# Performance work log

Hardware: AMD Instinct MI355X
Metric: run time of the kernel (lower is better)

Reference implementation:

```python
import jax, jax.numpy as jnp
import numpy as np

EMBED_DIM = 256
UNITS = 512


def setup_inputs() -> dict:
    key = jax.random.key(0)
    k1, k2, k3, k4, k5, k6, k7, k8 = jax.random.split(key, 8)
    B, L = 2048, 64
    features = jax.random.normal(k1, (B, L, EMBED_DIM), dtype=jnp.float32)
    hidden = jax.random.normal(k2, (B, UNITS), dtype=jnp.float32)
    s1 = 1.0 / np.sqrt(EMBED_DIM)
    s2 = 1.0 / np.sqrt(UNITS)
    W1 = jax.random.normal(k3, (EMBED_DIM, UNITS), dtype=jnp.float32) * s1
    b1 = jnp.zeros((UNITS,), dtype=jnp.float32)
    W2 = jax.random.normal(k4, (UNITS, UNITS), dtype=jnp.float32) * s2
    b2 = jnp.zeros((UNITS,), dtype=jnp.float32)
    V = jax.random.normal(k5, (UNITS, 1), dtype=jnp.float32) * s2
    bV = jnp.zeros((1,), dtype=jnp.float32)
    return {"features": features, "hidden": hidden, "W1": W1, "b1": b1,
            "W2": W2, "b2": b2, "V": V, "bV": bV}


def reference(features, hidden, W1, b1, W2, b2, V, bV):
    # features: [B, L, D_feat]; hidden: [B, U]
    # score = tanh(W1(features) + W2(hidden)[:, None])  -> [B, L, U]
    proj_f = jnp.einsum('bld,du->blu', features, W1) + b1
    proj_h = hidden @ W2 + b2                         # [B, U]
    score = jnp.tanh(proj_f + proj_h[:, None, :])     # [B, L, U]
    logits = jnp.einsum('blu,uo->blo', score, V) + bV  # [B, L, 1]
    attention_weights = jax.nn.softmax(logits, axis=1)  # softmax over L
    context_vector = jnp.sum(attention_weights * features, axis=1)  # [B, D_feat]
    return context_vector, attention_weights
```

## Files before the change

kernel.cpp:

```cpp
#include <hip/hip_runtime.h>
#include <math.h>

#define B_N 2048
#define L_N 64
#define D_N 256
#define U_N 512

typedef __attribute__((ext_vector_type(8))) short bf16x8;
typedef __attribute__((ext_vector_type(4))) float f32x4;

__device__ __forceinline__ float fast_tanh(float x) {
    float e = __builtin_amdgcn_exp2f(x * 2.8853900817779268f);
    float r = __builtin_amdgcn_rcpf(e + 1.0f);
    return fmaf(-2.0f, r, 1.0f);
}
__device__ __forceinline__ ushort f2bf(float x) {
    uint b = __float_as_uint(x);
    uint r = (b + 0x7FFF + ((b >> 16) & 1)) >> 16;
    return (ushort)r;
}
__device__ __forceinline__ float bf2f(ushort u) {
    uint v = ((uint)u) << 16;
    return __uint_as_float(v);
}

__global__ __launch_bounds__(256) void pack_weights(
    const float* __restrict__ W1, const float* __restrict__ W2,
    ushort* __restrict__ W1p, ushort* __restrict__ W2p)
{
    ushort tmp[8];
    if (blockIdx.x < 64) {
        int g = blockIdx.x * 256 + threadIdx.x;
        int ntg = g >> 9, ks = (g >> 6) & 7, lane = g & 63;
        int n  = ntg * 16 + (lane & 15);
        int kb = ks * 32 + (lane >> 4) * 8;
#pragma unroll
        for (int j = 0; j < 8; ++j) tmp[j] = f2bf(W1[(kb + j) * U_N + n]);
        *(uint4*)&W1p[(size_t)g * 8] = *(uint4*)tmp;
    } else {
        int g = (blockIdx.x - 64) * 256 + threadIdx.x;
        int ntg = g >> 10, ks = (g >> 6) & 15, lane = g & 63;
        int n  = ntg * 16 + (lane & 15);
        int kb = ks * 32 + (lane >> 4) * 8;
#pragma unroll
        for (int j = 0; j < 8; ++j) tmp[j] = f2bf(W2[(kb + j) * U_N + n]);
        *(uint4*)&W2p[(size_t)g * 8] = *(uint4*)tmp;
    }
}

__global__ __launch_bounds__(256) void proj_h_mfma(
    const float* __restrict__ hidden, const ushort* __restrict__ W2p,
    const float* __restrict__ b1, const float* __restrict__ b2,
    ushort* __restrict__ ph)
{
    __shared__ ushort As[16 * 512];

    const int t  = threadIdx.x;
    const int b0 = blockIdx.x * 16;
    const int u0 = blockIdx.y * 128;

#pragma unroll
    for (int i = 0; i < 4; ++i) {
        int f = t + i * 256;
        int m = f >> 6, c = f & 63;
        float4 x0 = *(const float4*)&hidden[(b0 + m) * U_N + c * 8];
        float4 x1 = *(const float4*)&hidden[(b0 + m) * U_N + c * 8 + 4];
        ushort tmp[8] = {f2bf(x0.x), f2bf(x0.y), f2bf(x0.z), f2bf(x0.w),
                         f2bf(x1.x), f2bf(x1.y), f2bf(x1.z), f2bf(x1.w)};
        *(uint4*)&As[(m * 64 + (c ^ (m & 7))) * 8] = *(uint4*)tmp;
    }
    __syncthreads();

    const int w = t >> 6, lane = t & 63;
    const int ml = lane & 15, q = lane >> 4;

    f32x4 acc[2];
#pragma unroll
    for (int nt = 0; nt < 2; ++nt) acc[nt] = (f32x4){0.f, 0.f, 0.f, 0.f};

    for (int ks = 0; ks < 16; ++ks) {
        int c = ks * 4 + q;
        bf16x8 a = *(const bf16x8*)&As[(ml * 64 + (c ^ (ml & 7))) * 8];
        bf16x8 bb[2];
#pragma unroll
        for (int nt = 0; nt < 2; ++nt) {
            int ntg = blockIdx.y * 8 + w * 2 + nt;
            bb[nt] = *(const bf16x8*)&W2p[(size_t)((ntg * 16 + ks) * 64 + lane) * 8];
        }
#pragma unroll
        for (int nt = 0; nt < 2; ++nt)
            acc[nt] = __builtin_amdgcn_mfma_f32_16x16x32_bf16(a, bb[nt], acc[nt], 0, 0, 0);
    }

#pragma unroll
    for (int nt = 0; nt < 2; ++nt) {
        int n = u0 + (w * 2 + nt) * 16 + ml;
        float bias = b1[n] + b2[n];
#pragma unroll
        for (int r = 0; r < 4; ++r)
            ph[(size_t)(b0 + q * 4 + r) * U_N + n] = f2bf(acc[nt][r] + bias);
    }
}

__global__ __launch_bounds__(256) void attn_kernel(
    const float* __restrict__ features, const ushort* __restrict__ W1p,
    const float* __restrict__ V, const float* __restrict__ bV,
    const ushort* __restrict__ ph, float* __restrict__ out)
{
    __shared__ ushort As[64 * 256];
    __shared__ float lpart[4][64];
    __shared__ float wls[64];

    const int b    = blockIdx.x;
    const int t    = threadIdx.x;
    const int w    = t >> 6;
    const int lane = t & 63;
    const int ml   = lane & 15;
    const int q    = lane >> 4;
    const float* fb = features + (size_t)b * (L_N * D_N);

#pragma unroll
    for (int i = 0; i < 8; ++i) {
        int f = t + i * 256;
        int m = f >> 5, c = f & 31;
        float4 x0 = *(const float4*)&fb[m * D_N + c * 8];
        float4 x1 = *(const float4*)&fb[m * D_N + c * 8 + 4];
        ushort tmp[8] = {f2bf(x0.x), f2bf(x0.y), f2bf(x0.z), f2bf(x0.w),
                         f2bf(x1.x), f2bf(x1.y), f2bf(x1.z), f2bf(x1.w)};
        *(uint4*)&As[(m * 32 + (c ^ (m & 31))) * 8] = *(uint4*)tmp;
    }
    __syncthreads();

    float lp[16];
#pragma unroll
    for (int j = 0; j < 16; ++j) lp[j] = 0.f;

    const ushort* W1w = W1p + (size_t)(w * 8) * 8 * 64 * 8;

    for (int uc = 0; uc < 4; ++uc) {
        f32x4 acc[4][2];
#pragma unroll
        for (int mt = 0; mt < 4; ++mt)
#pragma unroll
            for (int nt = 0; nt < 2; ++nt)
                acc[mt][nt] = (f32x4){0.f, 0.f, 0.f, 0.f};

        bf16x8 bfc[2], bfn[2];
#pragma unroll
        for (int nt = 0; nt < 2; ++nt)
            bfc[nt] = *(const bf16x8*)&W1w[(size_t)(((uc * 2 + nt) * 8 + 0) * 64 + lane) * 8];

        for (int ks = 0; ks < 8; ++ks) {
            if (ks < 7) {
#pragma unroll
                for (int nt = 0; nt < 2; ++nt)
                    bfn[nt] = *(const bf16x8*)&W1w[(size_t)(((uc * 2 + nt) * 8 + ks + 1) * 64 + lane) * 8];
            }
            bf16x8 a[4];
#pragma unroll
            for (int mt = 0; mt < 4; ++mt) {
                int m = mt * 16 + ml;
                int c = ks * 4 + q;
                a[mt] = *(const bf16x8*)&As[(m * 32 + (c ^ (m & 31))) * 8];
            }
#pragma unroll
            for (int nt = 0; nt < 2; ++nt)
#pragma unroll
                for (int mt = 0; mt < 4; ++mt)
                    acc[mt][nt] = __builtin_amdgcn_mfma_f32_16x16x32_bf16(
                        a[mt], bfc[nt], acc[mt][nt], 0, 0, 0);
            bfc[0] = bfn[0]; bfc[1] = bfn[1];
        }

#pragma unroll
        for (int nt = 0; nt < 2; ++nt) {
            int n = w * 128 + uc * 32 + nt * 16 + ml;
            float phv = bf2f(ph[(size_t)b * U_N + n]);
            float vv  = V[n];
#pragma unroll
            for (int mt = 0; mt < 4; ++mt)
#pragma unroll
                for (int r = 0; r < 4; ++r) {
                    float s = fast_tanh(acc[mt][nt][r] + phv);
                    lp[mt * 4 + r] = fmaf(s, vv, lp[mt * 4 + r]);
                }
        }
    }

#pragma unroll
    for (int off = 1; off <= 8; off <<= 1)
#pragma unroll
        for (int j = 0; j < 16; ++j)
            lp[j] += __shfl_xor(lp[j], off);
    if (ml == 0) {
#pragma unroll
        for (int mt = 0; mt < 4; ++mt)
#pragma unroll
            for (int r = 0; r < 4; ++r)
                lpart[w][mt * 16 + q * 4 + r] = lp[mt * 4 + r];
    }
    __syncthreads();

    if (t < 64) {
        float lsum = bV[0] + lpart[0][t] + lpart[1][t] + lpart[2][t] + lpart[3][t];
        float mx = lsum;
#pragma unroll
        for (int off = 32; off > 0; off >>= 1)
            mx = fmaxf(mx, __shfl_xor(mx, off));
        float e = __expf(lsum - mx);
        float ssum = e;
#pragma unroll
        for (int off = 32; off > 0; off >>= 1)
            ssum += __shfl_xor(ssum, off);
        float wt = e / ssum;
        wls[t] = wt;
        out[(size_t)B_N * D_N + (size_t)b * L_N + t] = wt;
    }
    __syncthreads();

    float ctx = 0.f;
#pragma unroll 16
    for (int l = 0; l < L_N; ++l) {
        ushort u = As[(l * 32 + ((t >> 3) ^ (l & 31))) * 8 + (t & 7)];
        ctx = fmaf(wls[l], bf2f(u), ctx);
    }
    out[(size_t)b * D_N + t] = ctx;
}

extern "C" void kernel_launch(void* const* d_in, const int* in_sizes, int n_in,
                              void* d_out, int out_size, void* d_ws, size_t ws_size,
                              hipStream_t stream) {
    const float* features = (const float*)d_in[0];
    const float* hidden   = (const float*)d_in[1];
    const float* W1       = (const float*)d_in[2];
    const float* b1       = (const float*)d_in[3];
    const float* W2       = (const float*)d_in[4];
    const float* b2       = (const float*)d_in[5];
    const float* V        = (const float*)d_in[6];
    const float* bV       = (const float*)d_in[7];
    float* out = (float*)d_out;

    ushort* ph  = (ushort*)d_ws;
    ushort* W1p = (ushort*)((char*)d_ws + (size_t)B_N * U_N * 2);
    ushort* W2p = (ushort*)((char*)d_ws + (size_t)B_N * U_N * 2 + (size_t)D_N * U_N * 2);

    pack_weights<<<192, 256, 0, stream>>>(W1, W2, W1p, W2p);
    proj_h_mfma<<<dim3(B_N / 16, U_N / 128), 256, 0, stream>>>(hidden, W2p, b1, b2, ph);
    attn_kernel<<<B_N, 256, 0, stream>>>(features, W1p, V, bV, ph, out);
}
```

Baseline: 262.8 us.

## Process several batches per block with double-buffered feature prefetch

Each attention block now handles four batch rows in turn. The features for the next row are loaded into registers while the current row's MFMA work runs, then written to a second LDS buffer, so global-load latency overlaps with compute. The W1 fragment prefetch is also deepened to two k-steps ahead. In exchange, LDS use doubles to 64KB per block, register pressure rises (16 float4 prefetch registers, with launch bounds set for 2 blocks per CU), and the grid shrinks to 512 blocks, which may leave compute units underfilled.

```diff
diff --git a/kernel.cpp b/kernel.cpp
--- a/kernel.cpp
+++ b/kernel.cpp
@@ -5,6 +5,7 @@
 #define L_N 64
 #define D_N 256
 #define U_N 512
+#define NB  4
 
 typedef __attribute__((ext_vector_type(8))) short bf16x8;
 typedef __attribute__((ext_vector_type(4))) float f32x4;
@@ -102,129 +103,164 @@
     }
 }
 
-__global__ __launch_bounds__(256) void attn_kernel(
+__global__ __launch_bounds__(256, 2) void attn_kernel(
     const float* __restrict__ features, const ushort* __restrict__ W1p,
     const float* __restrict__ V, const float* __restrict__ bV,
     const ushort* __restrict__ ph, float* __restrict__ out)
 {
-    __shared__ ushort As[64 * 256];
+    __shared__ ushort As[2][64 * 256];
     __shared__ float lpart[4][64];
     __shared__ float wls[64];
 
-    const int b    = blockIdx.x;
     const int t    = threadIdx.x;
     const int w    = t >> 6;
     const int lane = t & 63;
     const int ml   = lane & 15;
     const int q    = lane >> 4;
-    const float* fb = features + (size_t)b * (L_N * D_N);
-
-#pragma unroll
-    for (int i = 0; i < 8; ++i) {
-        int f = t + i * 256;
-        int m = f >> 5, c = f & 31;
-        float4 x0 = *(const float4*)&fb[m * D_N + c * 8];
-        float4 x1 = *(const float4*)&fb[m * D_N + c * 8 + 4];
-        ushort tmp[8] = {f2bf(x0.x), f2bf(x0.y), f2bf(x0.z), f2bf(x0.w),
-                         f2bf(x1.x), f2bf(x1.y), f2bf(x1.z), f2bf(x1.w)};
-        *(uint4*)&As[(m * 32 + (c ^ (m & 31))) * 8] = *(uint4*)tmp;
-    }
+    const int b0   = blockIdx.x * NB;
+
+    float4 pf[16];
+
+#define ISSUE(bb) do {                                                        \
+        const float* fb_ = features + (size_t)(bb) * (L_N * D_N);             \
+        _Pragma("unroll")                                                     \
+        for (int i = 0; i < 8; ++i) {                                         \
+            int f_ = t + i * 256;                                             \
+            int m_ = f_ >> 5, c_ = f_ & 31;                                   \
+            pf[2*i]   = *(const float4*)&fb_[m_ * D_N + c_ * 8];              \
+            pf[2*i+1] = *(const float4*)&fb_[m_ * D_N + c_ * 8 + 4];          \
+        }                                                                     \
+    } while (0)
+
+#define WRITE(buf) do {                                                       \
+        _Pragma("unroll")                                                     \
+        for (int i = 0; i < 8; ++i) {                                         \
+            int f_ = t + i * 256;                                             \
+            int m_ = f_ >> 5, c_ = f_ & 31;                                   \
+            float4 x0_ = pf[2*i], x1_ = pf[2*i+1];                            \
+            ushort tmp_[8] = {f2bf(x0_.x), f2bf(x0_.y), f2bf(x0_.z), f2bf(x0_.w), \
+                              f2bf(x1_.x), f2bf(x1_.y), f2bf(x1_.z), f2bf(x1_.w)}; \
+            *(uint4*)&As[buf][(m_ * 32 + (c_ ^ (m_ & 31))) * 8] = *(uint4*)tmp_;  \
+        }                                                                     \
+    } while (0)
+
+    ISSUE(b0);
+    WRITE(0);
     __syncthreads();
 
-    float lp[16];
-#pragma unroll
-    for (int j = 0; j < 16; ++j) lp[j] = 0.f;
-
     const ushort* W1w = W1p + (size_t)(w * 8) * 8 * 64 * 8;
-
-    for (int uc = 0; uc < 4; ++uc) {
-        f32x4 acc[4][2];
-#pragma unroll
-        for (int mt = 0; mt < 4; ++mt)
-#pragma unroll
-            for (int nt = 0; nt < 2; ++nt)
-                acc[mt][nt] = (f32x4){0.f, 0.f, 0.f, 0.f};
-
-        bf16x8 bfc[2], bfn[2];
-#pragma unroll
-        for (int nt = 0; nt < 2; ++nt)
-            bfc[nt] = *(const bf16x8*)&W1w[(size_t)(((uc * 2 + nt) * 8 + 0) * 64 + lane) * 8];
-
-        for (int ks = 0; ks < 8; ++ks) {
-            if (ks < 7) {
+    int cur = 0;
+
+    for (int bi = 0; bi < NB; ++bi) {
+        const int b = b0 + bi;
+
+        if (bi + 1 < NB) ISSUE(b + 1);
+        __builtin_amdgcn_sched_barrier(0);
+
+        float lp[16];
+#pragma unroll
+        for (int j = 0; j < 16; ++j) lp[j] = 0.f;
+
+        for (int uc = 0; uc < 4; ++uc) {
+            f32x4 acc[4][2];
+#pragma unroll
+            for (int mt = 0; mt < 4; ++mt)
 #pragma unroll
                 for (int nt = 0; nt < 2; ++nt)
-                    bfn[nt] = *(const bf16x8*)&W1w[(size_t)(((uc * 2 + nt) * 8 + ks + 1) * 64 + lane) * 8];
+                    acc[mt][nt] = (f32x4){0.f, 0.f, 0.f, 0.f};
+
+            bf16x8 bf0[2], bf1[2], bfn[2];
+#pragma unroll
+            for (int nt = 0; nt < 2; ++nt) {
+                bf0[nt] = *(const bf16x8*)&W1w[(size_t)(((uc * 2 + nt) * 8 + 0) * 64 + lane) * 8];
+                bf1[nt] = *(const bf16x8*)&W1w[(size_t)(((uc * 2 + nt) * 8 + 1) * 64 + lane) * 8];
             }
-            bf16x8 a[4];
-#pragma unroll
-            for (int mt = 0; mt < 4; ++mt) {
-                int m = mt * 16 + ml;
-                int c = ks * 4 + q;
-                a[mt] = *(const bf16x8*)&As[(m * 32 + (c ^ (m & 31))) * 8];
+
+            for (int ks = 0; ks < 8; ++ks) {
+                if (ks < 6) {
+#pragma unroll
+                    for (int nt = 0; nt < 2; ++nt)
+                        bfn[nt] = *(const bf16x8*)&W1w[(size_t)(((uc * 2 + nt) * 8 + ks + 2) * 64 + lane) * 8];
+                }
+                bf16x8 a[4];
+#pragma unroll
+                for (int mt = 0; mt < 4; ++mt) {
+                    int m = mt * 16 + ml;
+                    int c = ks * 4 + q;
+                    a[mt] = *(const bf16x8*)&As[cur][(m * 32 + (c ^ (m & 31))) * 8];
+                }
+#pragma unroll
+                for (int nt = 0; nt < 2; ++nt)
+#pragma unroll
+                    for (int mt = 0; mt < 4; ++mt)
+                        acc[mt][nt] = __builtin_amdgcn_mfma_f32_16x16x32_bf16(
+                            a[mt], bf0[nt], acc[mt][nt], 0, 0, 0);
+                bf0[0] = bf1[0]; bf0[1] = bf1[1];
+                bf1[0] = bfn[0]; bf1[1] = bfn[1];
             }
-#pragma unroll
-            for (int nt = 0; nt < 2; ++nt)
+
+#pragma unroll
+            for (int nt = 0; nt < 2; ++nt) {
+                int n = w * 128 + uc * 32 + nt * 16 + ml;
+                float phv = bf2f(ph[(size_t)b * U_N + n]);
+                float vv  = V[n];
 #pragma unroll
                 for (int mt = 0; mt < 4; ++mt)
-                    acc[mt][nt] = __builtin_amdgcn_mfma_f32_16x16x32_bf16(
-                        a[mt], bfc[nt], acc[mt][nt], 0, 0, 0);
-            bfc[0] = bfn[0]; bfc[1] = bfn[1];
-        }
-
-#pragma unroll
-        for (int nt = 0; nt < 2; ++nt) {
-            int n = w * 128 + uc * 32 + nt * 16 + ml;
-            float phv = bf2f(ph[(size_t)b * U_N + n]);
-            float vv  = V[n];
+#pragma unroll
+                    for (int r = 0; r < 4; ++r) {
+                        float s = fast_tanh(acc[mt][nt][r] + phv);
+                        lp[mt * 4 + r] = fmaf(s, vv, lp[mt * 4 + r]);
+                    }
+            }
+        }
+
+#pragma unroll
+        for (int off = 1; off <= 8; off <<= 1)
+#pragma unroll
+            for (int j = 0; j < 16; ++j)
+                lp[j] += __shfl_xor(lp[j], off);
+
+        __syncthreads();
+        if (bi + 1 < NB) WRITE(cur ^ 1);
+
+        if (ml == 0) {
 #pragma unroll
             for (int mt = 0; mt < 4; ++mt)
 #pragma unroll
-                for (int r = 0; r < 4; ++r) {
-                    float s = fast_tanh(acc[mt][nt][r] + phv);
-                    lp[mt * 4 + r] = fmaf(s, vv, lp[mt * 4 + r]);
-                }
-        }
-    }
-
-#pragma unroll
-    for (int off = 1; off <= 8; off <<= 1)
-#pragma unroll
-        for (int j = 0; j < 16; ++j)
-            lp[j] += __shfl_xor(lp[j], off);
-    if (ml == 0) {
-#pragma unroll
-        for (int mt = 0; mt < 4; ++mt)
-#pragma unroll
-            for (int r = 0; r < 4; ++r)
-                lpart[w][mt * 16 + q * 4 + r] = lp[mt * 4 + r];
-    }
-    __syncthreads();
-
-    if (t < 64) {
-        float lsum = bV[0] + lpart[0][t] + lpart[1][t] + lpart[2][t] + lpart[3][t];
-        float mx = lsum;
-#pragma unroll
-        for (int off = 32; off > 0; off >>= 1)
-            mx = fmaxf(mx, __shfl_xor(mx, off));
-        float e = __expf(lsum - mx);
-        float ssum = e;
-#pragma unroll
-        for (int off = 32; off > 0; off >>= 1)
-            ssum += __shfl_xor(ssum, off);
-        float wt = e / ssum;
-        wls[t] = wt;
-        out[(size_t)B_N * D_N + (size_t)b * L_N + t] = wt;
-    }
-    __syncthreads();
-
-    float ctx = 0.f;
+                for (int r = 0; r < 4; ++r)
+                    lpart[w][mt * 16 + q * 4 + r] = lp[mt * 4 + r];
+        }
+        __syncthreads();
+
+        if (t < 64) {
+            float lsum = bV[0] + lpart[0][t] + lpart[1][t] + lpart[2][t] + lpart[3][t];
+            float mx = lsum;
+#pragma unroll
+            for (int off = 32; off > 0; off >>= 1)
+                mx = fmaxf(mx, __shfl_xor(mx, off));
+            float e = __expf(lsum - mx);
+            float ssum = e;
+#pragma unroll
+            for (int off = 32; off > 0; off >>= 1)
+                ssum += __shfl_xor(ssum, off);
+            float wt = e / ssum;
+            wls[t] = wt;
+            out[(size_t)B_N * D_N + (size_t)b * L_N + t] = wt;
+        }
+        __syncthreads();
+
+        float ctx = 0.f;
 #pragma unroll 16
-    for (int l = 0; l < L_N; ++l) {
-        ushort u = As[(l * 32 + ((t >> 3) ^ (l & 31))) * 8 + (t & 7)];
-        ctx = fmaf(wls[l], bf2f(u), ctx);
-    }
-    out[(size_t)b * D_N + t] = ctx;
+        for (int l = 0; l < L_N; ++l) {
+            ushort u = As[cur][(l * 32 + ((t >> 3) ^ (l & 31))) * 8 + (t & 7)];
+            ctx = fmaf(wls[l], bf2f(u), ctx);
+        }
+        out[(size_t)b * D_N + t] = ctx;
+
+        cur ^= 1;
+    }
+#undef ISSUE
+#undef WRITE
 }
 
 extern "C" void kernel_launch(void* const* d_in, const int* in_sizes, int n_in,
@@ -246,5 +282,5 @@
 
     pack_weights<<<192, 256, 0, stream>>>(W1, W2, W1p, W2p);
     proj_h_mfma<<<dim3(B_N / 16, U_N / 128), 256, 0, stream>>>(hidden, W2p, b1, b2, ph);
-    attn_kernel<<<B_N, 256, 0, stream>>>(features, W1p, V, bV, ph, out);
-}
+    attn_kernel<<<B_N / NB, 256, 0, stream>>>(features, W1p, V, bV, ph, out);
+}
```

Measured after the change: 307.1 us. 16.8% more time.

## Pre-convert features to bf16 and double-buffer async LDS loads across batches

Applied to the files above, without the earlier changes.

Feature conversion to bf16 moves into the prep kernel, which writes a packed bf16 copy to the workspace. The attention kernel now handles 4 batches per block, prefetching the next batch's features into a second LDS buffer with global_load_lds while computing the current one. It also widens the per-wave N tile to 4 MFMA columns and fixes waves per EU at 2. The aim is to hide feature-load latency, at the cost of extra global traffic for the intermediate bf16 copy and doubled LDS.

```diff
diff --git a/kernel.cpp b/kernel.cpp
--- a/kernel.cpp
+++ b/kernel.cpp
@@ -5,6 +5,7 @@
 #define L_N 64
 #define D_N 256
 #define U_N 512
+#define NB  4
 
 typedef __attribute__((ext_vector_type(8))) short bf16x8;
 typedef __attribute__((ext_vector_type(4))) float f32x4;
@@ -24,27 +25,50 @@
     return __uint_as_float(v);
 }
 
-__global__ __launch_bounds__(256) void pack_weights(
+__device__ __forceinline__ void gll16(const ushort* g, ushort* l) {
+    __builtin_amdgcn_global_load_lds(
+        (const __attribute__((address_space(1))) unsigned int*)g,
+        (__attribute__((address_space(3))) unsigned int*)l,
+        16, 0, 0);
+}
+
+__global__ __launch_bounds__(256) void prep(
     const float* __restrict__ W1, const float* __restrict__ W2,
-    ushort* __restrict__ W1p, ushort* __restrict__ W2p)
+    const float* __restrict__ features,
+    ushort* __restrict__ W1p, ushort* __restrict__ W2p, ushort* __restrict__ fbf)
 {
-    ushort tmp[8];
+    const int t = threadIdx.x;
     if (blockIdx.x < 64) {
-        int g = blockIdx.x * 256 + threadIdx.x;
+        ushort tmp[8];
+        int g = blockIdx.x * 256 + t;
         int ntg = g >> 9, ks = (g >> 6) & 7, lane = g & 63;
         int n  = ntg * 16 + (lane & 15);
         int kb = ks * 32 + (lane >> 4) * 8;
 #pragma unroll
         for (int j = 0; j < 8; ++j) tmp[j] = f2bf(W1[(kb + j) * U_N + n]);
         *(uint4*)&W1p[(size_t)g * 8] = *(uint4*)tmp;
-    } else {
-        int g = (blockIdx.x - 64) * 256 + threadIdx.x;
+    } else if (blockIdx.x < 192) {
+        ushort tmp[8];
+        int g = (blockIdx.x - 64) * 256 + t;
         int ntg = g >> 10, ks = (g >> 6) & 15, lane = g & 63;
         int n  = ntg * 16 + (lane & 15);
         int kb = ks * 32 + (lane >> 4) * 8;
 #pragma unroll
         for (int j = 0; j < 8; ++j) tmp[j] = f2bf(W2[(kb + j) * U_N + n]);
         *(uint4*)&W2p[(size_t)g * 8] = *(uint4*)tmp;
+    } else {
+        int b = blockIdx.x - 192;
+        const float* fb = features + (size_t)b * (L_N * D_N);
+        ushort* fo = fbf + (size_t)b * (L_N * D_N);
+#pragma unroll
+        for (int i = 0; i < 8; ++i) {
+            int ch = t + i * 256;
+            float4 x0 = *(const float4*)&fb[ch * 8];
+            float4 x1 = *(const float4*)&fb[ch * 8 + 4];
+            ushort tv[8] = {f2bf(x0.x), f2bf(x0.y), f2bf(x0.z), f2bf(x0.w),
+                            f2bf(x1.x), f2bf(x1.y), f2bf(x1.z), f2bf(x1.w)};
+            *(uint4*)&fo[(size_t)ch * 8] = *(uint4*)tv;
+        }
     }
 }
 
@@ -102,129 +126,149 @@
     }
 }
 
-__global__ __launch_bounds__(256) void attn_kernel(
-    const float* __restrict__ features, const ushort* __restrict__ W1p,
+__global__ __launch_bounds__(256)
+__attribute__((amdgpu_waves_per_eu(2, 2)))
+void attn_kernel(
+    const ushort* __restrict__ fbf, const ushort* __restrict__ W1p,
     const float* __restrict__ V, const float* __restrict__ bV,
     const ushort* __restrict__ ph, float* __restrict__ out)
 {
-    __shared__ ushort As[64 * 256];
+    __shared__ ushort As[2][64 * 256];
     __shared__ float lpart[4][64];
     __shared__ float wls[64];
 
-    const int b    = blockIdx.x;
     const int t    = threadIdx.x;
     const int w    = t >> 6;
     const int lane = t & 63;
     const int ml   = lane & 15;
     const int q    = lane >> 4;
-    const float* fb = features + (size_t)b * (L_N * D_N);
-
-#pragma unroll
-    for (int i = 0; i < 8; ++i) {
-        int f = t + i * 256;
-        int m = f >> 5, c = f & 31;
-        float4 x0 = *(const float4*)&fb[m * D_N + c * 8];
-        float4 x1 = *(const float4*)&fb[m * D_N + c * 8 + 4];
-        ushort tmp[8] = {f2bf(x0.x), f2bf(x0.y), f2bf(x0.z), f2bf(x0.w),
-                         f2bf(x1.x), f2bf(x1.y), f2bf(x1.z), f2bf(x1.w)};
-        *(uint4*)&As[(m * 32 + (c ^ (m & 31))) * 8] = *(uint4*)tmp;
-    }
+    const int b0   = blockIdx.x * NB;
+
+#define ISSUE(bb, buf) do {                                                   \
+        const ushort* fb_ = fbf + (size_t)(bb) * (L_N * D_N);                 \
+        _Pragma("unroll")                                                     \
+        for (int i = 0; i < 8; ++i) {                                         \
+            int p0_ = w * 512 + i * 64;                     \
+            int p_  = p0_ + lane;                                             \
+            int m_  = p_ >> 5, cc_ = p_ & 31;                                 \
+            int s_  = m_ * 32 + (cc_ ^ (m_ & 31));                            \
+            gll16(fb_ + (size_t)s_ * 8, &As[buf][p0_ * 8]);                   \
+        }                                                                     \
+    } while (0)
+
+    ISSUE(b0, 0);
+    asm volatile("s_waitcnt vmcnt(0)" ::: "memory");
     __syncthreads();
 
-    float lp[16];
-#pragma unroll
-    for (int j = 0; j < 16; ++j) lp[j] = 0.f;
-
     const ushort* W1w = W1p + (size_t)(w * 8) * 8 * 64 * 8;
-
-    for (int uc = 0; uc < 4; ++uc) {
-        f32x4 acc[4][2];
-#pragma unroll
-        for (int mt = 0; mt < 4; ++mt)
-#pragma unroll
-            for (int nt = 0; nt < 2; ++nt)
-                acc[mt][nt] = (f32x4){0.f, 0.f, 0.f, 0.f};
-
-        bf16x8 bfc[2], bfn[2];
-#pragma unroll
-        for (int nt = 0; nt < 2; ++nt)
-            bfc[nt] = *(const bf16x8*)&W1w[(size_t)(((uc * 2 + nt) * 8 + 0) * 64 + lane) * 8];
-
-        for (int ks = 0; ks < 8; ++ks) {
-            if (ks < 7) {
-#pragma unroll
-                for (int nt = 0; nt < 2; ++nt)
-                    bfn[nt] = *(const bf16x8*)&W1w[(size_t)(((uc * 2 + nt) * 8 + ks + 1) * 64 + lane) * 8];
+    int cur = 0;
+
+    for (int bi = 0; bi < NB; ++bi) {
+        const int b = b0 + bi;
+
+        if (bi + 1 < NB) ISSUE(b + 1, cur ^ 1);
+
+        float lp[16];
+#pragma unroll
+        for (int j = 0; j < 16; ++j) lp[j] = 0.f;
+
+#pragma unroll
+        for (int uc = 0; uc < 2; ++uc) {
+            f32x4 acc[4][4];
+#pragma unroll
+            for (int mt = 0; mt < 4; ++mt)
+#pragma unroll
+                for (int nt = 0; nt < 4; ++nt)
+                    acc[mt][nt] = (f32x4){0.f, 0.f, 0.f, 0.f};
+
+            bf16x8 bfc[4], bfn[4];
+#pragma unroll
+            for (int nt = 0; nt < 4; ++nt)
+                bfc[nt] = *(const bf16x8*)&W1w[(size_t)(((uc * 4 + nt) * 8 + 0) * 64 + lane) * 8];
+
+            for (int ks = 0; ks < 8; ++ks) {
+                if (ks < 7) {
+#pragma unroll
+                    for (int nt = 0; nt < 4; ++nt)
+                        bfn[nt] = *(const bf16x8*)&W1w[(size_t)(((uc * 4 + nt) * 8 + ks + 1) * 64 + lane) * 8];
+                }
+                bf16x8 a[4];
+#pragma unroll
+                for (int mt = 0; mt < 4; ++mt) {
+                    int m = mt * 16 + ml;
+                    int c = ks * 4 + q;
+                    a[mt] = *(const bf16x8*)&As[cur][(m * 32 + (c ^ (m & 31))) * 8];
+                }
+#pragma unroll
+                for (int nt = 0; nt < 4; ++nt)
+#pragma unroll
+                    for (int mt = 0; mt < 4; ++mt)
+                        acc[mt][nt] = __builtin_amdgcn_mfma_f32_16x16x32_bf16(
+                            a[mt], bfc[nt], acc[mt][nt], 0, 0, 0);
+#pragma unroll
+                for (int nt = 0; nt < 4; ++nt) bfc[nt] = bfn[nt];
             }
-            bf16x8 a[4];
-#pragma unroll
-            for (int mt = 0; mt < 4; ++mt) {
-                int m = mt * 16 + ml;
-                int c = ks * 4 + q;
-                a[mt] = *(const bf16x8*)&As[(m * 32 + (c ^ (m & 31))) * 8];
+
+#pragma unroll
+            for (int nt = 0; nt < 4; ++nt) {
+                int n = w * 128 + uc * 64 + nt * 16 + ml;
+                float phv = bf2f(ph[(size_t)b * U_N + n]);
+                float vv  = V[n];
+#pragma unroll
+                for (int mt = 0; mt < 4; ++mt)
+#pragma unroll
+                    for (int r = 0; r < 4; ++r) {
+                        float s = fast_tanh(acc[mt][nt][r] + phv);
+                        lp[mt * 4 + r] = fmaf(s, vv, lp[mt * 4 + r]);
+                    }
             }
-#pragma unroll
-            for (int nt = 0; nt < 2; ++nt)
-#pragma unroll
-                for (int mt = 0; mt < 4; ++mt)
-                    acc[mt][nt] = __builtin_amdgcn_mfma_f32_16x16x32_bf16(
-                        a[mt], bfc[nt], acc[mt][nt], 0, 0, 0);
-            bfc[0] = bfn[0]; bfc[1] = bfn[1];
-        }
-
-#pragma unroll
-        for (int nt = 0; nt < 2; ++nt) {
-            int n = w * 128 + uc * 32 + nt * 16 + ml;
-            float phv = bf2f(ph[(size_t)b * U_N + n]);
-            float vv  = V[n];
+        }
+
+#pragma unroll
+        for (int off = 1; off <= 8; off <<= 1)
+#pragma unroll
+            for (int j = 0; j < 16; ++j)
+                lp[j] += __shfl_xor(lp[j], off);
+
+        if (ml == 0) {
 #pragma unroll
             for (int mt = 0; mt < 4; ++mt)
 #pragma unroll
-                for (int r = 0; r < 4; ++r) {
-                    float s = fast_tanh(acc[mt][nt][r] + phv);
-                    lp[mt * 4 + r] = fmaf(s, vv, lp[mt * 4 + r]);
-                }
-        }
-    }
-
-#pragma unroll
-    for (int off = 1; off <= 8; off <<= 1)
-#pragma unroll
-        for (int j = 0; j < 16; ++j)
-            lp[j] += __shfl_xor(lp[j], off);
-    if (ml == 0) {
-#pragma unroll
-        for (int mt = 0; mt < 4; ++mt)
-#pragma unroll
-            for (int r = 0; r < 4; ++r)
-                lpart[w][mt * 16 + q * 4 + r] = lp[mt * 4 + r];
-    }
-    __syncthreads();
-
-    if (t < 64) {
-        float lsum = bV[0] + lpart[0][t] + lpart[1][t] + lpart[2][t] + lpart[3][t];
-        float mx = lsum;
-#pragma unroll
-        for (int off = 32; off > 0; off >>= 1)
-            mx = fmaxf(mx, __shfl_xor(mx, off));
-        float e = __expf(lsum - mx);
-        float ssum = e;
-#pragma unroll
-        for (int off = 32; off > 0; off >>= 1)
-            ssum += __shfl_xor(ssum, off);
-        float wt = e / ssum;
-        wls[t] = wt;
-        out[(size_t)B_N * D_N + (size_t)b * L_N + t] = wt;
-    }
-    __syncthreads();
-
-    float ctx = 0.f;
+                for (int r = 0; r < 4; ++r)
+                    lpart[w][mt * 16 + q * 4 + r] = lp[mt * 4 + r];
+        }
+        __syncthreads();
+
+        if (t < 64) {
+            float lsum = bV[0] + lpart[0][t] + lpart[1][t] + lpart[2][t] + lpart[3][t];
+            float mx = lsum;
+#pragma unroll
+            for (int off = 32; off > 0; off >>= 1)
+                mx = fmaxf(mx, __shfl_xor(mx, off));
+            float e = __expf(lsum - mx);
+            float ssum = e;
+#pragma unroll
+            for (int off = 32; off > 0; off >>= 1)
+                ssum += __shfl_xor(ssum, off);
+            float wt = e / ssum;
+            wls[t] = wt;
+            out[(size_t)B_N * D_N + (size_t)b * L_N + t] = wt;
+        }
+        __syncthreads();
+
+        float ctx = 0.f;
 #pragma unroll 16
-    for (int l = 0; l < L_N; ++l) {
-        ushort u = As[(l * 32 + ((t >> 3) ^ (l & 31))) * 8 + (t & 7)];
-        ctx = fmaf(wls[l], bf2f(u), ctx);
-    }
-    out[(size_t)b * D_N + t] = ctx;
+        for (int l = 0; l < L_N; ++l) {
+            ushort u = As[cur][(l * 32 + ((t >> 3) ^ (l & 31))) * 8 + (t & 7)];
+            ctx = fmaf(wls[l], bf2f(u), ctx);
+        }
+        out[(size_t)b * D_N + t] = ctx;
+
+        asm volatile("s_waitcnt vmcnt(0)" ::: "memory");
+        __syncthreads();
+        cur ^= 1;
+    }
+#undef ISSUE
 }
 
 extern "C" void kernel_launch(void* const* d_in, const int* in_sizes, int n_in,
@@ -243,8 +287,10 @@
     ushort* ph  = (ushort*)d_ws;
     ushort* W1p = (ushort*)((char*)d_ws + (size_t)B_N * U_N * 2);
     ushort* W2p = (ushort*)((char*)d_ws + (size_t)B_N * U_N * 2 + (size_t)D_N * U_N * 2);
-
-    pack_weights<<<192, 256, 0, stream>>>(W1, W2, W1p, W2p);
+    ushort* fbf = (ushort*)((char*)d_ws + (size_t)B_N * U_N * 2 + (size_t)D_N * U_N * 2
+                                        + (size_t)U_N * U_N * 2);
+
+    prep<<<192 + B_N, 256, 0, stream>>>(W1, W2, features, W1p, W2p, fbf);
     proj_h_mfma<<<dim3(B_N / 16, U_N / 128), 256, 0, stream>>>(hidden, W2p, b1, b2, ph);
-    attn_kernel<<<B_N, 256, 0, stream>>>(features, W1p, V, bV, ph, out);
-}
+    attn_kernel<<<B_N / NB, 256, 0, stream>>>(fbf, W1p, V, bV, ph, out);
+}
```

Measured after the change: 402.6 us. 1.53x slower.

## Process four batches per block with async global-to-LDS feature prefetch

Applied to the files above, without the earlier changes.

The attention kernel now handles four batch rows per block. Feature rows are staged through an fp32 LDS buffer using global_load_lds, in two halves, so loading the next half or batch overlaps the MFMA and tanh work on the current one. The grid shrinks fourfold and the added 32 KB fp32 staging buffer raises LDS use per block, which can lower occupancy. The extra barriers and the reduced number of blocks may limit how much latency this hides.

```diff
diff --git a/kernel.cpp b/kernel.cpp
--- a/kernel.cpp
+++ b/kernel.cpp
@@ -5,6 +5,7 @@
 #define L_N 64
 #define D_N 256
 #define U_N 512
+#define NB  4
 
 typedef __attribute__((ext_vector_type(8))) short bf16x8;
 typedef __attribute__((ext_vector_type(4))) float f32x4;
@@ -22,6 +23,13 @@
 __device__ __forceinline__ float bf2f(ushort u) {
     uint v = ((uint)u) << 16;
     return __uint_as_float(v);
+}
+
+__device__ __forceinline__ void gll16(const float* g, float* l) {
+    __builtin_amdgcn_global_load_lds(
+        (const __attribute__((address_space(1))) unsigned int*)g,
+        (__attribute__((address_space(3))) unsigned int*)l,
+        16, 0, 0);
 }
 
 __global__ __launch_bounds__(256) void pack_weights(
@@ -108,123 +116,153 @@
     const ushort* __restrict__ ph, float* __restrict__ out)
 {
     __shared__ ushort As[64 * 256];
-    __shared__ float lpart[4][64];
-    __shared__ float wls[64];
-
-    const int b    = blockIdx.x;
+    __shared__ float  S[32 * 256];
+    __shared__ float  lpart[4][64];
+    __shared__ float  wls[64];
+
     const int t    = threadIdx.x;
     const int w    = t >> 6;
     const int lane = t & 63;
     const int ml   = lane & 15;
     const int q    = lane >> 4;
-    const float* fb = features + (size_t)b * (L_N * D_N);
-
-#pragma unroll
-    for (int i = 0; i < 8; ++i) {
-        int f = t + i * 256;
-        int m = f >> 5, c = f & 31;
-        float4 x0 = *(const float4*)&fb[m * D_N + c * 8];
-        float4 x1 = *(const float4*)&fb[m * D_N + c * 8 + 4];
-        ushort tmp[8] = {f2bf(x0.x), f2bf(x0.y), f2bf(x0.z), f2bf(x0.w),
-                         f2bf(x1.x), f2bf(x1.y), f2bf(x1.z), f2bf(x1.w)};
-        *(uint4*)&As[(m * 32 + (c ^ (m & 31))) * 8] = *(uint4*)tmp;
-    }
+    const int b0   = blockIdx.x * NB;
+
+#define ISSUE_HALF(bb_, hh) do {                                              \
+        const float* fsrc_ = features + (size_t)(bb_) * (L_N * D_N)           \
+                             + ((hh) * 32 + w * 8) * D_N;                     \
+        _Pragma("unroll")                                                     \
+        for (int i_ = 0; i_ < 8; ++i_)                                        \
+            gll16(fsrc_ + i_ * D_N + lane * 4, &S[w * 2048 + i_ * 256]);      \
+    } while (0)
+
+#define CONV_HALF(hh) do {                                                    \
+        _Pragma("unroll")                                                     \
+        for (int i_ = 0; i_ < 8; ++i_) {                                      \
+            float4 x_ = *(const float4*)&S[w * 2048 + i_ * 256 + lane * 4];   \
+            ushort tv_[4] = {f2bf(x_.x), f2bf(x_.y), f2bf(x_.z), f2bf(x_.w)}; \
+            int m_ = (hh) * 32 + w * 8 + i_, c_ = lane >> 1;                  \
+            *(uint2*)&As[(m_ * 32 + (c_ ^ (m_ & 31))) * 8 + (lane & 1) * 4]   \
+                = *(uint2*)tv_;                                               \
+        }                                                                     \
+    } while (0)
+
+#define HALFPASS(hh, b_) do {                                                 \
+        for (int uc = 0; uc < 4; ++uc) {                                      \
+            f32x4 acc[2][2];                                                  \
+            _Pragma("unroll")                                                 \
+            for (int mt = 0; mt < 2; ++mt)                                    \
+                _Pragma("unroll")                                             \
+                for (int nt = 0; nt < 2; ++nt)                                \
+                    acc[mt][nt] = (f32x4){0.f, 0.f, 0.f, 0.f};                \
+            for (int ks = 0; ks < 8; ++ks) {                                  \
+                bf16x8 bb[2];                                                 \
+                _Pragma("unroll")                                             \
+                for (int nt = 0; nt < 2; ++nt)                                \
+                    bb[nt] = *(const bf16x8*)&W1w[(size_t)(((uc * 2 + nt) * 8 + ks) * 64 + lane) * 8]; \
+                _Pragma("unroll")                                             \
+                for (int mt = 0; mt < 2; ++mt) {                              \
+                    int m_ = (hh) * 32 + mt * 16 + ml, c_ = ks * 4 + q;       \
+                    bf16x8 av = *(const bf16x8*)&As[(m_ * 32 + (c_ ^ (m_ & 31))) * 8]; \
+                    _Pragma("unroll")                                         \
+                    for (int nt = 0; nt < 2; ++nt)                            \
+                        acc[mt][nt] = __builtin_amdgcn_mfma_f32_16x16x32_bf16( \
+                            av, bb[nt], acc[mt][nt], 0, 0, 0);                \
+                }                                                             \
+            }                                                                 \
+            _Pragma("unroll")                                                 \
+            for (int nt = 0; nt < 2; ++nt) {                                  \
+                int n_ = w * 128 + uc * 32 + nt * 16 + ml;                    \
+                float phv_ = bf2f(ph[(size_t)(b_) * U_N + n_]);               \
+                float vv_  = V[n_];                                           \
+                _Pragma("unroll")                                             \
+                for (int mt = 0; mt < 2; ++mt)                                \
+                    _Pragma("unroll")                                         \
+                    for (int r = 0; r < 4; ++r) {                             \
+                        float s_ = fast_tanh(acc[mt][nt][r] + phv_);          \
+                        lp[(hh) * 8 + mt * 4 + r] = fmaf(s_, vv_, lp[(hh) * 8 + mt * 4 + r]); \
+                    }                                                         \
+            }                                                                 \
+        }                                                                     \
+    } while (0)
+
+    const ushort* W1w = W1p + (size_t)(w * 8) * 8 * 64 * 8;
+
+    ISSUE_HALF(b0, 0);
+    asm volatile("s_waitcnt vmcnt(0)" ::: "memory");
+    CONV_HALF(0);
+    ISSUE_HALF(b0, 1);
     __syncthreads();
 
-    float lp[16];
-#pragma unroll
-    for (int j = 0; j < 16; ++j) lp[j] = 0.f;
-
-    const ushort* W1w = W1p + (size_t)(w * 8) * 8 * 64 * 8;
-
-    for (int uc = 0; uc < 4; ++uc) {
-        f32x4 acc[4][2];
-#pragma unroll
-        for (int mt = 0; mt < 4; ++mt)
-#pragma unroll
-            for (int nt = 0; nt < 2; ++nt)
-                acc[mt][nt] = (f32x4){0.f, 0.f, 0.f, 0.f};
-
-        bf16x8 bfc[2], bfn[2];
-#pragma unroll
-        for (int nt = 0; nt < 2; ++nt)
-            bfc[nt] = *(const bf16x8*)&W1w[(size_t)(((uc * 2 + nt) * 8 + 0) * 64 + lane) * 8];
-
-        for (int ks = 0; ks < 8; ++ks) {
-            if (ks < 7) {
-#pragma unroll
-                for (int nt = 0; nt < 2; ++nt)
-                    bfn[nt] = *(const bf16x8*)&W1w[(size_t)(((uc * 2 + nt) * 8 + ks + 1) * 64 + lane) * 8];
-            }
-            bf16x8 a[4];
-#pragma unroll
-            for (int mt = 0; mt < 4; ++mt) {
-                int m = mt * 16 + ml;
-                int c = ks * 4 + q;
-                a[mt] = *(const bf16x8*)&As[(m * 32 + (c ^ (m & 31))) * 8];
-            }
-#pragma unroll
-            for (int nt = 0; nt < 2; ++nt)
-#pragma unroll
-                for (int mt = 0; mt < 4; ++mt)
-                    acc[mt][nt] = __builtin_amdgcn_mfma_f32_16x16x32_bf16(
-                        a[mt], bfc[nt], acc[mt][nt], 0, 0, 0);
-            bfc[0] = bfn[0]; bfc[1] = bfn[1];
-        }
-
-#pragma unroll
-        for (int nt = 0; nt < 2; ++nt) {
-            int n = w * 128 + uc * 32 + nt * 16 + ml;
-            float phv = bf2f(ph[(size_t)b * U_N + n]);
-            float vv  = V[n];
-#pragma unroll
-            for (int mt = 0; mt < 4; ++mt)
-#pragma unroll
-                for (int r = 0; r < 4; ++r) {
-                    float s = fast_tanh(acc[mt][nt][r] + phv);
-                    lp[mt * 4 + r] = fmaf(s, vv, lp[mt * 4 + r]);
-                }
-        }
-    }
-
-#pragma unroll
-    for (int off = 1; off <= 8; off <<= 1)
-#pragma unroll
-        for (int j = 0; j < 16; ++j)
-            lp[j] += __shfl_xor(lp[j], off);
-    if (ml == 0) {
-#pragma unroll
-        for (int mt = 0; mt < 4; ++mt)
-#pragma unroll
-            for (int r = 0; r < 4; ++r)
-                lpart[w][mt * 16 + q * 4 + r] = lp[mt * 4 + r];
-    }
-    __syncthreads();
-
-    if (t < 64) {
-        float lsum = bV[0] + lpart[0][t] + lpart[1][t] + lpart[2][t] + lpart[3][t];
-        float mx = lsum;
-#pragma unroll
-        for (int off = 32; off > 0; off >>= 1)
-            mx = fmaxf(mx, __shfl_xor(mx, off));
-        float e = __expf(lsum - mx);
-        float ssum = e;
-#pragma unroll
-        for (int off = 32; off > 0; off >>= 1)
-            ssum += __shfl_xor(ssum, off);
-        float wt = e / ssum;
-        wls[t] = wt;
-        out[(size_t)B_N * D_N + (size_t)b * L_N + t] = wt;
-    }
-    __syncthreads();
-
-    float ctx = 0.f;
+    for (int bi = 0; bi < NB; ++bi) {
+        const int b = b0 + bi;
+        const bool pre = (bi + 1 < NB);
+
+        float lp[16];
+#pragma unroll
+        for (int j = 0; j < 16; ++j) lp[j] = 0.f;
+
+        HALFPASS(0, b);
+
+        asm volatile("s_waitcnt vmcnt(0)" ::: "memory");
+        CONV_HALF(1);
+        if (pre) ISSUE_HALF(b + 1, 0);
+        __syncthreads();
+
+        HALFPASS(1, b);
+
+#pragma unroll
+        for (int off = 1; off <= 8; off <<= 1)
+#pragma unroll
+            for (int j = 0; j < 16; ++j)
+                lp[j] += __shfl_xor(lp[j], off);
+
+        if (ml == 0) {
+#pragma unroll
+            for (int hh = 0; hh < 2; ++hh)
+#pragma unroll
+                for (int mt = 0; mt < 2; ++mt)
+#pragma unroll
+                    for (int r = 0; r < 4; ++r)
+                        lpart[w][hh * 32 + mt * 16 + q * 4 + r] = lp[hh * 8 + mt * 4 + r];
+        }
+        __syncthreads();
+
+        if (t < 64) {
+            float lsum = bV[0] + lpart[0][t] + lpart[1][t] + lpart[2][t] + lpart[3][t];
+            float mx = lsum;
+#pragma unroll
+            for (int off = 32; off > 0; off >>= 1)
+                mx = fmaxf(mx, __shfl_xor(mx, off));
+            float e = __expf(lsum - mx);
+            float ssum = e;
+#pragma unroll
+            for (int off = 32; off > 0; off >>= 1)
+                ssum += __shfl_xor(ssum, off);
+            float wt = e / ssum;
+            wls[t] = wt;
+            out[(size_t)B_N * D_N + (size_t)b * L_N + t] = wt;
+        }
+        __syncthreads();
+
+        float ctx = 0.f;
 #pragma unroll 16
-    for (int l = 0; l < L_N; ++l) {
-        ushort u = As[(l * 32 + ((t >> 3) ^ (l & 31))) * 8 + (t & 7)];
-        ctx = fmaf(wls[l], bf2f(u), ctx);
-    }
-    out[(size_t)b * D_N + t] = ctx;
+        for (int l = 0; l < L_N; ++l) {
+            ushort u = As[(l * 32 + ((t >> 3) ^ (l & 31))) * 8 + (t & 7)];
+            ctx = fmaf(wls[l], bf2f(u), ctx);
+        }
+        out[(size_t)b * D_N + t] = ctx;
+        __syncthreads();
+
+        if (pre) {
+            asm volatile("s_waitcnt vmcnt(0)" ::: "memory");
+            CONV_HALF(0);
+            ISSUE_HALF(b + 1, 1);
+        }
+        __syncthreads();
+    }
+#undef ISSUE_HALF
+#undef CONV_HALF
+#undef HALFPASS
 }
 
 extern "C" void kernel_launch(void* const* d_in, const int* in_sizes, int n_in,
@@ -246,5 +284,5 @@
 
     pack_weights<<<192, 256, 0, stream>>>(W1, W2, W1p, W2p);
     proj_h_mfma<<<dim3(B_N / 16, U_N / 128), 256, 0, stream>>>(hidden, W2p, b1, b2, ph);
-    attn_kernel<<<B_N, 256, 0, stream>>>(features, W1p, V, bV, ph, out);
-}
+    attn_kernel<<<B_N / NB, 256, 0, stream>>>(features, W1p, V, bV, ph, out);
+}
```

After: 265.5 us. No clear change (+1.0%).
